# Performance work log

Hardware: AMD Instinct MI355X
Metric: run time of the kernel (lower is better)

Reference implementation:

```python
import jax, jax.numpy as jnp
import numpy as np

N_NODES = 50000
N_EDGES = 800000
NODE = 128
EDGE = 16
H = 96
OUT = 64
L = 3
BN_EPS = 1e-5


def setup_inputs() -> dict:
    key = jax.random.key(0)
    ks = iter(jax.random.split(key, 48))
    def rn(shape, s=0.05):
        return jax.random.normal(next(ks), shape, dtype=jnp.float32) * s
    inp = {
        "x": jax.random.normal(next(ks), (N_NODES, NODE), dtype=jnp.float32),
        "edge_index": jax.random.randint(next(ks), (2, N_EDGES), 0, N_NODES, dtype=jnp.int32),
        "edge_attr": jax.random.normal(next(ks), (N_EDGES, EDGE), dtype=jnp.float32),
        # GCNConv (layer 0)
        "gcn_lin_w": rn((NODE, H)), "gcn_lin_b": rn((H,)),
        "gcn_root": rn((1, H)),
        "gcn_bw1": rn((EDGE, H)), "gcn_bb1": rn((H,)),
        "gcn_bw2": rn((H, H)), "gcn_bb2": rn((H,)),
        # GINConv layers 1..L-1 (stacked)
        "gin_bw1": rn((L - 1, EDGE, H)), "gin_bb1": rn((L - 1, H)),
        "gin_bw2": rn((L - 1, H, H)), "gin_bb2": rn((L - 1, H)),
        "gin_mw1": rn((L - 1, H, H)), "gin_mb1": rn((L - 1, H)),
        "gin_mw2": rn((L - 1, H, H)), "gin_mb2": rn((L - 1, H)),
        "gin_eps": jnp.zeros((L - 1,), jnp.float32),
        # BatchNorm (eval mode, running stats)
        "bn_gamma": jnp.ones((L, H), jnp.float32),
        "bn_beta": jnp.zeros((L, H), jnp.float32),
        "bn_mean": rn((L, H)),
        "bn_var": jnp.ones((L, H), jnp.float32) + jax.random.uniform(next(ks), (L, H), dtype=jnp.float32) * 0.1,
        # head
        "fc1_w": rn((L * H, H)), "fc1_b": rn((H,)),
        "fc2_w": rn((H, OUT)), "fc2_b": rn((OUT,)),
    }
    return inp


def _bn(x, gamma, beta, mean, var):
    return (x - mean) * jax.lax.rsqrt(var + BN_EPS) * gamma + beta


def reference(x, edge_index, edge_attr,
              gcn_lin_w, gcn_lin_b, gcn_root, gcn_bw1, gcn_bb1, gcn_bw2, gcn_bb2,
              gin_bw1, gin_bb1, gin_bw2, gin_bb2, gin_mw1, gin_mb1, gin_mw2, gin_mb2, gin_eps,
              bn_gamma, bn_beta, bn_mean, bn_var,
              fc1_w, fc1_b, fc2_w, fc2_b):
    n = x.shape[0]
    row, col = edge_index[0], edge_index[1]  # source, target

    # ---- Layer 0: GCNConv with edge attributes ----
    h = x @ gcn_lin_w + gcn_lin_b                                    # [N,H]
    ee = jax.nn.relu(edge_attr @ gcn_bw1 + gcn_bb1) @ gcn_bw2 + gcn_bb2  # [E,H]
    deg = jax.ops.segment_sum(jnp.ones_like(row, dtype=h.dtype), row, num_segments=n) + 1.0
    dinv = jax.lax.rsqrt(deg)                                        # deg >= 1, no inf
    norm = dinv[row] * dinv[col]                                     # [E]
    msg = norm[:, None] * jax.nn.relu(h[row] + ee)                   # [E,H]
    agg = jax.ops.segment_sum(msg, col, num_segments=n)              # [N,H]
    h = agg + jax.nn.relu(h + gcn_root) / deg[:, None]
    h = _bn(jax.nn.relu(h), bn_gamma[0], bn_beta[0], bn_mean[0], bn_var[0])
    feats = [h]

    # ---- Layers 1..L-1: GINConv with edge attributes ----
    for i in range(L - 1):
        ee = jax.nn.relu(edge_attr @ gin_bw1[i] + gin_bb1[i]) @ gin_bw2[i] + gin_bb2[i]  # [E,H]
        agg = jax.ops.segment_sum(jax.nn.relu(h[row] + ee), col, num_segments=n)          # [N,H]
        z = (1.0 + gin_eps[i]) * h + agg
        z = jax.nn.relu(z @ gin_mw1[i] + gin_mb1[i]) @ gin_mw2[i] + gin_mb2[i]
        h = _bn(jax.nn.relu(z), bn_gamma[i + 1], bn_beta[i + 1], bn_mean[i + 1], bn_var[i + 1])
        feats.append(h)

    cat = jnp.concatenate(feats, axis=-1)                            # [N, L*H]
    y = jax.nn.relu(cat @ fc1_w + fc1_b)                             # dropout is eval-mode identity
    return y @ fc2_w + fc2_b                                         # [N, OUT]
```

## Files before the change

kernel.cpp:

```cpp
#include <hip/hip_runtime.h>


#define HH 96
#define EDGEF 16
#define CAT (3 * HH)

typedef __attribute__((ext_vector_type(8))) short bf16x8;
typedef __attribute__((ext_vector_type(4))) float f32x4;
typedef __attribute__((ext_vector_type(4))) unsigned short ubf16x4;

__device__ __forceinline__ unsigned short f2bf(float f) {
    unsigned u = __float_as_uint(f);
    u += 0x7fffu + ((u >> 16) & 1u);
    return (unsigned short)(u >> 16);
}
__device__ __forceinline__ float bf2f(unsigned short s) {
    return __uint_as_float(((unsigned)s) << 16);
}

template <int K, int F, int AMODE, int EPI>
__global__ __launch_bounds__(256) void node_gemm(
    const void* __restrict__ Aptr, int lda,
    const float* __restrict__ agg,
    const float* __restrict__ eps_arr, int li,
    const float* __restrict__ W, const float* __restrict__ bias,
    void* __restrict__ Cptr, int ldc,
    unsigned short* __restrict__ bf_copy,
    const float* __restrict__ gamma, const float* __restrict__ beta,
    const float* __restrict__ mean, const float* __restrict__ var,
    int M)
{
    constexpr int SW = ((K * 2) % 128 == 0) ? 7 : 3;
    constexpr int NFT = F / 16;
    __shared__ __align__(16) short s_wt[F * K];

    const int tid = threadIdx.x;
    const int lane = tid & 63;
    const int w = tid >> 6;
    const int lr = lane & 15;
    const int lg = lane >> 4;

    for (int idx = tid; idx < F * K; idx += 256) {
        int f = idx / K, k = idx - f * K;
        s_wt[idx ^ ((f & SW) << 3)] = (short)f2bf(W[k * F + f]);
    }
    __syncthreads();

    const int R0 = blockIdx.x * 64 + 16 * w;
    const int Ra = min(R0 + lr, M - 1);

    float e1 = 0.f;
    if (AMODE == 2) e1 = 1.f + eps_arr[li];

    f32x4 acc[NFT];
#pragma unroll
    for (int ft = 0; ft < NFT; ++ft) {
        float b = bias[16 * ft + lr];
        acc[ft][0] = b; acc[ft][1] = b; acc[ft][2] = b; acc[ft][3] = b;
    }

#pragma unroll
    for (int kt = 0; kt < K / 32; ++kt) {
        bf16x8 ae;
        if (AMODE == 0) {
            const float* ap = (const float*)Aptr + (size_t)Ra * lda + 32 * kt + 8 * lg;
            f32x4 a0 = *(const f32x4*)ap;
            f32x4 a1 = *(const f32x4*)(ap + 4);
#pragma unroll
            for (int j = 0; j < 4; ++j) {
                ae[j] = (short)f2bf(a0[j]); ae[4 + j] = (short)f2bf(a1[j]);
            }
        } else if (AMODE == 1) {
            ae = *(const bf16x8*)((const unsigned short*)Aptr + (size_t)Ra * lda + 32 * kt + 8 * lg);
        } else {
            const unsigned short* hp = (const unsigned short*)Aptr + (size_t)Ra * lda + 32 * kt + 8 * lg;
            bf16x8 h8 = *(const bf16x8*)hp;
            const float* gp = agg + (size_t)Ra * HH + 32 * kt + 8 * lg;
            f32x4 g0 = *(const f32x4*)gp;
            f32x4 g1 = *(const f32x4*)(gp + 4);
#pragma unroll
            for (int j = 0; j < 4; ++j) {
                ae[j]     = (short)f2bf(fmaf(e1, bf2f((unsigned short)h8[j]), g0[j]));
                ae[4 + j] = (short)f2bf(fmaf(e1, bf2f((unsigned short)h8[4 + j]), g1[j]));
            }
        }
#pragma unroll
        for (int ft = 0; ft < NFT; ++ft) {
            bf16x8 bw = *(const bf16x8*)&s_wt[((lr + 16 * ft) * K + 32 * kt + 8 * lg) ^ ((lr & SW) << 3)];
            acc[ft] = __builtin_amdgcn_mfma_f32_16x16x32_bf16(ae, bw, acc[ft], 0, 0, 0);
        }
    }

    float scale[NFT], shiftv[NFT];
    if (EPI == 2) {
#pragma unroll
        for (int ft = 0; ft < NFT; ++ft) {
            int col = 16 * ft + lr;
            float s = gamma[col] * rsqrtf(var[col] + 1e-5f);
            scale[ft] = s;
            shiftv[ft] = beta[col] - mean[col] * s;
        }
    }
#pragma unroll
    for (int reg = 0; reg < 4; ++reg) {
        int r = R0 + 4 * lg + reg;
        if (r < M) {
#pragma unroll
            for (int ft = 0; ft < NFT; ++ft) {
                int col = 16 * ft + lr;
                float v = acc[ft][reg];
                if (EPI == 0) {
                    ((float*)Cptr)[(size_t)r * ldc + col] = v;
                } else if (EPI == 1) {
                    ((unsigned short*)Cptr)[(size_t)r * ldc + col] = f2bf(fmaxf(v, 0.f));
                } else if (EPI == 2) {
                    float z = fmaxf(v, 0.f) * scale[ft] + shiftv[ft];
                    unsigned short zb = f2bf(z);
                    ((unsigned short*)Cptr)[(size_t)r * ldc + col] = zb;
                    bf_copy[(size_t)r * F + col] = zb;
                } else {
                    ((float*)Cptr)[(size_t)r * ldc + col] = v;
                    bf_copy[(size_t)r * F + col] = f2bf(v);
                }
            }
        }
    }
}

__global__ void init_kernel(float* __restrict__ deg, int* __restrict__ cnt, int N)
{
    int i = blockIdx.x * blockDim.x + threadIdx.x;
    if (i < N) { deg[i] = 1.f; cnt[i] = 0; }
}

__global__ void count_kernel(const int* __restrict__ row, const int* __restrict__ col,
                             float* __restrict__ deg, int* __restrict__ cnt, int E)
{
    int e = blockIdx.x * blockDim.x + threadIdx.x;
    if (e < E) {
        atomicAdd(&deg[row[e]], 1.f);
        atomicAdd(&cnt[col[e]], 1);
    }
}

__global__ void scan1_kernel(const int* __restrict__ cnt, int* __restrict__ start,
                             int* __restrict__ bsum, int N)
{
    __shared__ int s[256];
    int tid = threadIdx.x;
    int i = blockIdx.x * 256 + tid;
    int v = (i < N) ? cnt[i] : 0;
    s[tid] = v;
    __syncthreads();
#pragma unroll
    for (int off = 1; off < 256; off <<= 1) {
        int t = (tid >= off) ? s[tid - off] : 0;
        __syncthreads();
        s[tid] += t;
        __syncthreads();
    }
    if (i < N) start[i] = s[tid] - v;
    if (tid == 255) bsum[blockIdx.x] = s[255];
}

__global__ void scan2_kernel(int* __restrict__ bsum, int nb)
{
    __shared__ int s[256];
    int tid = threadIdx.x;
    int v = (tid < nb) ? bsum[tid] : 0;
    s[tid] = v;
    __syncthreads();
#pragma unroll
    for (int off = 1; off < 256; off <<= 1) {
        int t = (tid >= off) ? s[tid - off] : 0;
        __syncthreads();
        s[tid] += t;
        __syncthreads();
    }
    if (tid < nb) bsum[tid] = s[tid] - v;
}

__global__ void scan3_kernel(int* __restrict__ start, const int* __restrict__ bsum,
                             int* __restrict__ cursor,
                             const float* __restrict__ deg, float* __restrict__ dinv,
                             int N, int E)
{
    int i = blockIdx.x * blockDim.x + threadIdx.x;
    if (i < N) {
        int f = start[i] + bsum[i >> 8];
        start[i] = f;
        cursor[i] = f;
        dinv[i] = rsqrtf(deg[i]);
    } else if (i == N) {
        start[N] = E;
    }
}

__global__ void scatter_ea_kernel(const int* __restrict__ row, const int* __restrict__ col,
                                  int* __restrict__ cursor,
                                  const float* __restrict__ ea,
                                  int* __restrict__ row_sorted,
                                  unsigned short* __restrict__ eas, int E)
{
    int e = blockIdx.x * blockDim.x + threadIdx.x;
    if (e >= E) return;
    int c = col[e];
    int p = atomicAdd(&cursor[c], 1);
    row_sorted[p] = row[e];
    const float* src = ea + (size_t)e * EDGEF;
    f32x4 v0 = *(const f32x4*)(src);
    f32x4 v1 = *(const f32x4*)(src + 4);
    f32x4 v2 = *(const f32x4*)(src + 8);
    f32x4 v3 = *(const f32x4*)(src + 12);
    bf16x8 o0, o1;
#pragma unroll
    for (int j = 0; j < 4; ++j) {
        o0[j] = (short)f2bf(v0[j]); o0[4 + j] = (short)f2bf(v1[j]);
        o1[j] = (short)f2bf(v2[j]); o1[4 + j] = (short)f2bf(v3[j]);
    }
    *(bf16x8*)(eas + (size_t)p * EDGEF) = o0;
    *(bf16x8*)(eas + (size_t)p * EDGEF + 8) = o1;
}

template <bool GCN>
__global__ __launch_bounds__(256, 4) void edge_kernel(
    const unsigned short* __restrict__ ea_sorted,
    const int* __restrict__ row_sorted,
    const int* __restrict__ seg_start,
    const float* __restrict__ bw1, const float* __restrict__ bb1,
    const float* __restrict__ bw2, const float* __restrict__ bb2,
    const unsigned short* __restrict__ hbf,
    const float* __restrict__ dinv,
    float* __restrict__ agg,
    int N)
{
    __shared__ __align__(16) short s_bw2T[96][104];
    __shared__ __align__(16) short s_bw1T[96][16];
    __shared__ __align__(16) short s_t[4][16][104];
    __shared__ float s_bias[192];

    const int tid = threadIdx.x;
    const int lane = tid & 63;
    const int w = tid >> 6;
    const int lr = lane & 15;
    const int lg = lane >> 4;

    for (int idx = tid; idx < HH * HH; idx += 256) {
        int k = idx / HH, f = idx - k * HH;
        s_bw2T[f][k] = (short)f2bf(bw2[idx]);
    }
    for (int idx = tid; idx < EDGEF * HH; idx += 256) {
        int k = idx / HH, f = idx - k * HH;
        s_bw1T[f][k] = (short)f2bf(bw1[idx]);
    }
    if (tid < HH) { s_bias[tid] = bb1[tid]; s_bias[HH + tid] = bb2[tid]; }
    __syncthreads();

    const f32x4 zf = {0.f, 0.f, 0.f, 0.f};
    const int nwaves = gridDim.x * 4;

    for (int c = blockIdx.x * 4 + w; c < N; c += nwaves) {
        const int s0 = seg_start[c];
        const int s1 = seg_start[c + 1];
        float dinv_c = GCN ? dinv[c] : 1.f;

        f32x4 acc[6];
#pragma unroll
        for (int ft = 0; ft < 6; ++ft) acc[ft] = zf;

        for (int b = s0; b < s1; b += 16) {
            const int epos = b + lr;
            const bool vld = (epos < s1);
            const int epc = vld ? epos : s0;
            const int r = row_sorted[epc];

            const unsigned short* hrow = hbf + (size_t)r * HH + 24 * lg;
            bf16x8 h0 = *(const bf16x8*)(hrow);
            bf16x8 h1 = *(const bf16x8*)(hrow + 8);
            bf16x8 h2 = *(const bf16x8*)(hrow + 16);

            float nrm = GCN ? dinv[r] * dinv_c : 1.f;

            bf16x8 ae;
#pragma unroll
            for (int j = 0; j < 8; ++j) ae[j] = 0;
            if (lg < 2)
                ae = *(const bf16x8*)(ea_sorted + (size_t)epc * EDGEF + 8 * lg);

#pragma unroll
            for (int ft = 0; ft < 6; ++ft) {
                bf16x8 b1;
#pragma unroll
                for (int j = 0; j < 8; ++j) b1[j] = 0;
                if (lg < 2)
                    b1 = *(const bf16x8*)&s_bw1T[lr + 16 * ft][8 * lg];
                f32x4 tacc = __builtin_amdgcn_mfma_f32_16x16x32_bf16(ae, b1, zf, 0, 0, 0);
                float bsv = s_bias[lr + 16 * ft];
#pragma unroll
                for (int reg = 0; reg < 4; ++reg) {
                    float v = fmaxf(tacc[reg] + bsv, 0.f);
                    s_t[w][4 * lg + reg][lr + 16 * ft] = (short)f2bf(v);
                }
            }
            __builtin_amdgcn_wave_barrier();

            bf16x8 bt[3];
#pragma unroll
            for (int kt = 0; kt < 3; ++kt)
                bt[kt] = *(const bf16x8*)&s_t[w][lr][8 * lg + 32 * kt];
            __builtin_amdgcn_wave_barrier();

            *(bf16x8*)&s_t[w][lr][24 * lg]      = h0;
            *(bf16x8*)&s_t[w][lr][24 * lg + 8]  = h1;
            *(bf16x8*)&s_t[w][lr][24 * lg + 16] = h2;
            __builtin_amdgcn_wave_barrier();

#pragma unroll
            for (int ft = 0; ft < 6; ++ft) {
                f32x4 ee = zf;
#pragma unroll
                for (int kt = 0; kt < 3; ++kt) {
                    bf16x8 aw = *(const bf16x8*)&s_bw2T[lr + 16 * ft][8 * lg + 32 * kt];
                    ee = __builtin_amdgcn_mfma_f32_16x16x32_bf16(aw, bt[kt], ee, 0, 0, 0);
                }
                const int fb = 16 * ft + 4 * lg;
                f32x4 bb = *(const f32x4*)&s_bias[HH + fb];
                ubf16x4 hv = *(const ubf16x4*)&s_t[w][lr][fb];
#pragma unroll
                for (int reg = 0; reg < 4; ++reg) {
                    float m = fmaxf(bf2f(hv[reg]) + ee[reg] + bb[reg], 0.f) * nrm;
                    acc[ft][reg] += vld ? m : 0.f;
                }
            }
        }

#pragma unroll
        for (int ft = 0; ft < 6; ++ft) {
#pragma unroll
            for (int reg = 0; reg < 4; ++reg) {
                float v = acc[ft][reg];
                v += __shfl_xor(v, 1);
                v += __shfl_xor(v, 2);
                v += __shfl_xor(v, 4);
                v += __shfl_xor(v, 8);
                acc[ft][reg] = v;
            }
        }
        if (lr == 0) {
#pragma unroll
            for (int ft = 0; ft < 6; ++ft)
                *(f32x4*)&agg[(size_t)c * HH + 16 * ft + 4 * lg] = acc[ft];
        }
    }
}

__global__ void gcn_epilogue_kernel(
    const float* __restrict__ agg, const float* __restrict__ hbuf,
    const float* __restrict__ root, const float* __restrict__ deg,
    const float* __restrict__ gamma, const float* __restrict__ beta,
    const float* __restrict__ mean, const float* __restrict__ var,
    unsigned short* __restrict__ featsbf, unsigned short* __restrict__ hb, int N)
{
    int idx = blockIdx.x * blockDim.x + threadIdx.x;
    if (idx >= N * (HH / 4)) return;
    int n = idx / (HH / 4), q = idx - n * (HH / 4);
    int f0 = 4 * q;
    f32x4 a  = *(const f32x4*)&agg[(size_t)n * HH + f0];
    f32x4 h  = *(const f32x4*)&hbuf[(size_t)n * HH + f0];
    f32x4 rt = *(const f32x4*)&root[f0];
    f32x4 gm = *(const f32x4*)&gamma[f0];
    f32x4 bt = *(const f32x4*)&beta[f0];
    f32x4 mn = *(const f32x4*)&mean[f0];
    f32x4 vr = *(const f32x4*)&var[f0];
    float di = 1.f / deg[n];
    ubf16x4 o;
#pragma unroll
    for (int j = 0; j < 4; ++j) {
        float self = fmaxf(h[j] + rt[j], 0.f) * di;
        float v = fmaxf(a[j] + self, 0.f);
        v = (v - mn[j]) * rsqrtf(vr[j] + 1e-5f) * gm[j] + bt[j];
        o[j] = f2bf(v);
    }
    *(ubf16x4*)&featsbf[(size_t)n * CAT + f0] = o;
    *(ubf16x4*)&hb[(size_t)n * HH + f0] = o;
}

extern "C" void kernel_launch(void* const* d_in, const int* in_sizes, int n_in,
                              void* d_out, int out_size, void* d_ws, size_t ws_size,
                              hipStream_t stream)
{
    const float* x         = (const float*)d_in[0];
    const int*   eidx      = (const int*)d_in[1];
    const float* edge_attr = (const float*)d_in[2];
    const float* gcn_lin_w = (const float*)d_in[3];
    const float* gcn_lin_b = (const float*)d_in[4];
    const float* gcn_root  = (const float*)d_in[5];
    const float* gcn_bw1   = (const float*)d_in[6];
    const float* gcn_bb1   = (const float*)d_in[7];
    const float* gcn_bw2   = (const float*)d_in[8];
    const float* gcn_bb2   = (const float*)d_in[9];
    const float* gin_bw1   = (const float*)d_in[10];
    const float* gin_bb1   = (const float*)d_in[11];
    const float* gin_bw2   = (const float*)d_in[12];
    const float* gin_bb2   = (const float*)d_in[13];
    const float* gin_mw1   = (const float*)d_in[14];
    const float* gin_mb1   = (const float*)d_in[15];
    const float* gin_mw2   = (const float*)d_in[16];
    const float* gin_mb2   = (const float*)d_in[17];
    const float* gin_eps   = (const float*)d_in[18];
    const float* bn_gamma  = (const float*)d_in[19];
    const float* bn_beta   = (const float*)d_in[20];
    const float* bn_mean   = (const float*)d_in[21];
    const float* bn_var    = (const float*)d_in[22];
    const float* fc1_w     = (const float*)d_in[23];
    const float* fc1_b     = (const float*)d_in[24];
    const float* fc2_w     = (const float*)d_in[25];
    const float* fc2_b     = (const float*)d_in[26];
    float* out = (float*)d_out;

    const int N = in_sizes[0] / 128;
    const int E = in_sizes[1] / 2;
    const int* row = eidx;
    const int* col = eidx + E;

    char* ws = (char*)d_ws;
    float* deg        = (float*)(ws);
    float* dinv       = (float*)(ws + (size_t)256 * 1024);
    int*   seg_start  = (int*)(ws + (size_t)512 * 1024);
    int*   cursor     = (int*)(ws + (size_t)768 * 1024);
    int*   bsum       = (int*)(ws + (size_t)1024 * 1024);
    int*   row_sorted = (int*)(ws + (size_t)1088 * 1024);
    unsigned short* ea_sorted = (unsigned short*)(ws + (size_t)8 * 1024 * 1024);
    unsigned short* hb        = (unsigned short*)(ws + (size_t)34 * 1024 * 1024);
    float* hbuf   = (float*)(ws + (size_t)44 * 1024 * 1024);
    float* agg    = (float*)(ws + (size_t)64 * 1024 * 1024);
    unsigned short* featsbf = (unsigned short*)(ws + (size_t)84 * 1024 * 1024);
    unsigned short* z1bf    = (unsigned short*)(ws + (size_t)113 * 1024 * 1024);
    unsigned short* r1bf    = (unsigned short*)(ws + (size_t)123 * 1024 * 1024);

    const int ew_blocks = 1024;
    const int q_grid = (N * (HH / 4) + 255) / 256;
    const int gemm_grid = (N + 63) / 64;
    const int e_grid = (E + 255) / 256;
    const int n_grid = (N + 255) / 256;
    const int nchunks = (N + 255) / 256;

    init_kernel<<<n_grid, 256, 0, stream>>>(deg, cursor, N);
    count_kernel<<<e_grid, 256, 0, stream>>>(row, col, deg, cursor, E);
    scan1_kernel<<<nchunks, 256, 0, stream>>>(cursor, seg_start, bsum, N);
    scan2_kernel<<<1, 256, 0, stream>>>(bsum, nchunks);
    scan3_kernel<<<(N + 256) / 256, 256, 0, stream>>>(seg_start, bsum, cursor, deg, dinv, N, E);
    scatter_ea_kernel<<<e_grid, 256, 0, stream>>>(row, col, cursor, edge_attr,
                                                  row_sorted, ea_sorted, E);

    node_gemm<128, 96, 0, 3><<<gemm_grid, 256, 0, stream>>>(
        x, 128, nullptr, nullptr, 0, gcn_lin_w, gcn_lin_b,
        hbuf, HH, hb, nullptr, nullptr, nullptr, nullptr, N);
    edge_kernel<true><<<ew_blocks, 256, 0, stream>>>(
        ea_sorted, row_sorted, seg_start,
        gcn_bw1, gcn_bb1, gcn_bw2, gcn_bb2, hb, dinv, agg, N);
    gcn_epilogue_kernel<<<q_grid, 256, 0, stream>>>(
        agg, hbuf, gcn_root, deg, bn_gamma, bn_beta, bn_mean, bn_var, featsbf, hb, N);

    for (int i = 0; i < 2; ++i) {
        edge_kernel<false><<<ew_blocks, 256, 0, stream>>>(
            ea_sorted, row_sorted, seg_start,
            gin_bw1 + (size_t)i * EDGEF * HH, gin_bb1 + i * HH,
            gin_bw2 + (size_t)i * HH * HH, gin_bb2 + i * HH,
            hb, dinv, agg, N);
        node_gemm<96, 96, 2, 1><<<gemm_grid, 256, 0, stream>>>(
            hb, HH, agg, gin_eps, i,
            gin_mw1 + (size_t)i * HH * HH, gin_mb1 + i * HH,
            z1bf, HH, nullptr, nullptr, nullptr, nullptr, nullptr, N);
        node_gemm<96, 96, 1, 2><<<gemm_grid, 256, 0, stream>>>(
            z1bf, HH, nullptr, nullptr, 0,
            gin_mw2 + (size_t)i * HH * HH, gin_mb2 + i * HH,
            featsbf + (i + 1) * HH, CAT, hb,
            bn_gamma + (i + 1) * HH, bn_beta + (i + 1) * HH,
            bn_mean + (i + 1) * HH, bn_var + (i + 1) * HH, N);
    }

    node_gemm<288, 96, 1, 1><<<gemm_grid, 256, 0, stream>>>(
        featsbf, CAT, nullptr, nullptr, 0, fc1_w, fc1_b,
        r1bf, HH, nullptr, nullptr, nullptr, nullptr, nullptr, N);
    node_gemm<96, 64, 1, 0><<<gemm_grid, 256, 0, stream>>>(
        r1bf, HH, nullptr, nullptr, 0, fc2_w, fc2_b,
        out, 64, nullptr, nullptr, nullptr, nullptr, nullptr, N);
}
```

Measured before the change: 696.9 us.

## Use packed bf16 conversions and enlarge edge kernel blocks to 1024 threads

Replaces per-element manual fp32-to-bf16 rounding with packed two-element conversions via hip_bfloat162 across several kernels. Reconfigures the edge kernel to 1024-thread blocks (16 waves) with 512 blocks, so shared weights are staged once per larger block. It also folds the second bias into the MFMA accumulator init and replaces the conditional add with a masked FMA. The larger block raises LDS use per block and the launch bound of 1024,8 may limit registers per thread, which could cause spills.

```diff
diff --git a/kernel.cpp b/kernel.cpp
--- a/kernel.cpp
+++ b/kernel.cpp
@@ -1,4 +1,5 @@
 #include <hip/hip_runtime.h>
+#include <hip/hip_bf16.h>
 
 
 #define HH 96
@@ -8,6 +9,9 @@
 typedef __attribute__((ext_vector_type(8))) short bf16x8;
 typedef __attribute__((ext_vector_type(4))) float f32x4;
 typedef __attribute__((ext_vector_type(4))) unsigned short ubf16x4;
+
+typedef union { bf16x8 v; unsigned u[4]; } bfpack8;
+typedef union { ubf16x4 v; unsigned u[2]; } bfpack4;
 
 __device__ __forceinline__ unsigned short f2bf(float f) {
     unsigned u = __float_as_uint(f);
@@ -16,6 +20,10 @@
 }
 __device__ __forceinline__ float bf2f(unsigned short s) {
     return __uint_as_float(((unsigned)s) << 16);
+}
+__device__ __forceinline__ unsigned pkbf2(float lo, float hi) {
+    __hip_bfloat162 b = __float22bfloat162_rn(make_float2(lo, hi));
+    union { __hip_bfloat162 b2; unsigned u; } cv; cv.b2 = b; return cv.u;
 }
 
 template <int K, int F, int AMODE, int EPI>
@@ -66,10 +74,10 @@
             const float* ap = (const float*)Aptr + (size_t)Ra * lda + 32 * kt + 8 * lg;
             f32x4 a0 = *(const f32x4*)ap;
             f32x4 a1 = *(const f32x4*)(ap + 4);
-#pragma unroll
-            for (int j = 0; j < 4; ++j) {
-                ae[j] = (short)f2bf(a0[j]); ae[4 + j] = (short)f2bf(a1[j]);
-            }
+            bfpack8 p;
+            p.u[0] = pkbf2(a0[0], a0[1]); p.u[1] = pkbf2(a0[2], a0[3]);
+            p.u[2] = pkbf2(a1[0], a1[1]); p.u[3] = pkbf2(a1[2], a1[3]);
+            ae = p.v;
         } else if (AMODE == 1) {
             ae = *(const bf16x8*)((const unsigned short*)Aptr + (size_t)Ra * lda + 32 * kt + 8 * lg);
         } else {
@@ -78,11 +86,18 @@
             const float* gp = agg + (size_t)Ra * HH + 32 * kt + 8 * lg;
             f32x4 g0 = *(const f32x4*)gp;
             f32x4 g1 = *(const f32x4*)(gp + 4);
-#pragma unroll
-            for (int j = 0; j < 4; ++j) {
-                ae[j]     = (short)f2bf(fmaf(e1, bf2f((unsigned short)h8[j]), g0[j]));
-                ae[4 + j] = (short)f2bf(fmaf(e1, bf2f((unsigned short)h8[4 + j]), g1[j]));
-            }
+            float t0 = fmaf(e1, bf2f((unsigned short)h8[0]), g0[0]);
+            float t1 = fmaf(e1, bf2f((unsigned short)h8[1]), g0[1]);
+            float t2 = fmaf(e1, bf2f((unsigned short)h8[2]), g0[2]);
+            float t3 = fmaf(e1, bf2f((unsigned short)h8[3]), g0[3]);
+            float t4 = fmaf(e1, bf2f((unsigned short)h8[4]), g1[0]);
+            float t5 = fmaf(e1, bf2f((unsigned short)h8[5]), g1[1]);
+            float t6 = fmaf(e1, bf2f((unsigned short)h8[6]), g1[2]);
+            float t7 = fmaf(e1, bf2f((unsigned short)h8[7]), g1[3]);
+            bfpack8 p;
+            p.u[0] = pkbf2(t0, t1); p.u[1] = pkbf2(t2, t3);
+            p.u[2] = pkbf2(t4, t5); p.u[3] = pkbf2(t6, t7);
+            ae = p.v;
         }
 #pragma unroll
         for (int ft = 0; ft < NFT; ++ft) {
@@ -212,18 +227,17 @@
     f32x4 v1 = *(const f32x4*)(src + 4);
     f32x4 v2 = *(const f32x4*)(src + 8);
     f32x4 v3 = *(const f32x4*)(src + 12);
-    bf16x8 o0, o1;
-#pragma unroll
-    for (int j = 0; j < 4; ++j) {
-        o0[j] = (short)f2bf(v0[j]); o0[4 + j] = (short)f2bf(v1[j]);
-        o1[j] = (short)f2bf(v2[j]); o1[4 + j] = (short)f2bf(v3[j]);
-    }
-    *(bf16x8*)(eas + (size_t)p * EDGEF) = o0;
-    *(bf16x8*)(eas + (size_t)p * EDGEF + 8) = o1;
+    bfpack8 o0, o1;
+    o0.u[0] = pkbf2(v0[0], v0[1]); o0.u[1] = pkbf2(v0[2], v0[3]);
+    o0.u[2] = pkbf2(v1[0], v1[1]); o0.u[3] = pkbf2(v1[2], v1[3]);
+    o1.u[0] = pkbf2(v2[0], v2[1]); o1.u[1] = pkbf2(v2[2], v2[3]);
+    o1.u[2] = pkbf2(v3[0], v3[1]); o1.u[3] = pkbf2(v3[2], v3[3]);
+    *(bf16x8*)(eas + (size_t)p * EDGEF) = o0.v;
+    *(bf16x8*)(eas + (size_t)p * EDGEF + 8) = o1.v;
 }
 
 template <bool GCN>
-__global__ __launch_bounds__(256, 4) void edge_kernel(
+__global__ __launch_bounds__(1024, 8) void edge_kernel(
     const unsigned short* __restrict__ ea_sorted,
     const int* __restrict__ row_sorted,
     const int* __restrict__ seg_start,
@@ -236,7 +250,7 @@
 {
     __shared__ __align__(16) short s_bw2T[96][104];
     __shared__ __align__(16) short s_bw1T[96][16];
-    __shared__ __align__(16) short s_t[4][16][104];
+    __shared__ __align__(16) short s_t[16][16][104];
     __shared__ float s_bias[192];
 
     const int tid = threadIdx.x;
@@ -245,11 +259,11 @@
     const int lr = lane & 15;
     const int lg = lane >> 4;
 
-    for (int idx = tid; idx < HH * HH; idx += 256) {
+    for (int idx = tid; idx < HH * HH; idx += 1024) {
         int k = idx / HH, f = idx - k * HH;
         s_bw2T[f][k] = (short)f2bf(bw2[idx]);
     }
-    for (int idx = tid; idx < EDGEF * HH; idx += 256) {
+    for (int idx = tid; idx < EDGEF * HH; idx += 1024) {
         int k = idx / HH, f = idx - k * HH;
         s_bw1T[f][k] = (short)f2bf(bw1[idx]);
     }
@@ -257,9 +271,9 @@
     __syncthreads();
 
     const f32x4 zf = {0.f, 0.f, 0.f, 0.f};
-    const int nwaves = gridDim.x * 4;
-
-    for (int c = blockIdx.x * 4 + w; c < N; c += nwaves) {
+    const int nwaves = gridDim.x * 16;
+
+    for (int c = blockIdx.x * 16 + w; c < N; c += nwaves) {
         const int s0 = seg_start[c];
         const int s1 = seg_start[c + 1];
         float dinv_c = GCN ? dinv[c] : 1.f;
@@ -279,7 +293,7 @@
             bf16x8 h1 = *(const bf16x8*)(hrow + 8);
             bf16x8 h2 = *(const bf16x8*)(hrow + 16);
 
-            float nrm = GCN ? dinv[r] * dinv_c : 1.f;
+            const float msk = vld ? (GCN ? dinv[r] * dinv_c : 1.f) : 0.f;
 
             bf16x8 ae;
 #pragma unroll
@@ -296,11 +310,17 @@
                     b1 = *(const bf16x8*)&s_bw1T[lr + 16 * ft][8 * lg];
                 f32x4 tacc = __builtin_amdgcn_mfma_f32_16x16x32_bf16(ae, b1, zf, 0, 0, 0);
                 float bsv = s_bias[lr + 16 * ft];
-#pragma unroll
-                for (int reg = 0; reg < 4; ++reg) {
-                    float v = fmaxf(tacc[reg] + bsv, 0.f);
-                    s_t[w][4 * lg + reg][lr + 16 * ft] = (short)f2bf(v);
-                }
+                float v0 = fmaxf(tacc[0] + bsv, 0.f);
+                float v1 = fmaxf(tacc[1] + bsv, 0.f);
+                float v2 = fmaxf(tacc[2] + bsv, 0.f);
+                float v3 = fmaxf(tacc[3] + bsv, 0.f);
+                unsigned u01 = pkbf2(v0, v1);
+                unsigned u23 = pkbf2(v2, v3);
+                const int colf = lr + 16 * ft;
+                s_t[w][4 * lg + 0][colf] = (short)u01;
+                s_t[w][4 * lg + 1][colf] = (short)(u01 >> 16);
+                s_t[w][4 * lg + 2][colf] = (short)u23;
+                s_t[w][4 * lg + 3][colf] = (short)(u23 >> 16);
             }
             __builtin_amdgcn_wave_barrier();
 
@@ -317,19 +337,18 @@
 
 #pragma unroll
             for (int ft = 0; ft < 6; ++ft) {
-                f32x4 ee = zf;
+                const int fb = 16 * ft + 4 * lg;
+                f32x4 ee = *(const f32x4*)&s_bias[HH + fb];
 #pragma unroll
                 for (int kt = 0; kt < 3; ++kt) {
                     bf16x8 aw = *(const bf16x8*)&s_bw2T[lr + 16 * ft][8 * lg + 32 * kt];
                     ee = __builtin_amdgcn_mfma_f32_16x16x32_bf16(aw, bt[kt], ee, 0, 0, 0);
                 }
-                const int fb = 16 * ft + 4 * lg;
-                f32x4 bb = *(const f32x4*)&s_bias[HH + fb];
                 ubf16x4 hv = *(const ubf16x4*)&s_t[w][lr][fb];
 #pragma unroll
                 for (int reg = 0; reg < 4; ++reg) {
-                    float m = fmaxf(bf2f(hv[reg]) + ee[reg] + bb[reg], 0.f) * nrm;
-                    acc[ft][reg] += vld ? m : 0.f;
+                    float m = fmaxf(bf2f(hv[reg]) + ee[reg], 0.f);
+                    acc[ft][reg] = fmaf(m, msk, acc[ft][reg]);
                 }
             }
         }
@@ -373,16 +392,18 @@
     f32x4 mn = *(const f32x4*)&mean[f0];
     f32x4 vr = *(const f32x4*)&var[f0];
     float di = 1.f / deg[n];
-    ubf16x4 o;
+    float vv[4];
 #pragma unroll
     for (int j = 0; j < 4; ++j) {
         float self = fmaxf(h[j] + rt[j], 0.f) * di;
         float v = fmaxf(a[j] + self, 0.f);
-        v = (v - mn[j]) * rsqrtf(vr[j] + 1e-5f) * gm[j] + bt[j];
-        o[j] = f2bf(v);
-    }
-    *(ubf16x4*)&featsbf[(size_t)n * CAT + f0] = o;
-    *(ubf16x4*)&hb[(size_t)n * HH + f0] = o;
+        vv[j] = (v - mn[j]) * rsqrtf(vr[j] + 1e-5f) * gm[j] + bt[j];
+    }
+    bfpack4 o;
+    o.u[0] = pkbf2(vv[0], vv[1]);
+    o.u[1] = pkbf2(vv[2], vv[3]);
+    *(ubf16x4*)&featsbf[(size_t)n * CAT + f0] = o.v;
+    *(ubf16x4*)&hb[(size_t)n * HH + f0] = o.v;
 }
 
 extern "C" void kernel_launch(void* const* d_in, const int* in_sizes, int n_in,
@@ -438,7 +459,7 @@
     unsigned short* z1bf    = (unsigned short*)(ws + (size_t)113 * 1024 * 1024);
     unsigned short* r1bf    = (unsigned short*)(ws + (size_t)123 * 1024 * 1024);
 
-    const int ew_blocks = 1024;
+    const int ew_blocks = 512;
     const int q_grid = (N * (HH / 4) + 255) / 256;
     const int gemm_grid = (N + 63) / 64;
     const int e_grid = (E + 255) / 256;
@@ -456,14 +477,14 @@
     node_gemm<128, 96, 0, 3><<<gemm_grid, 256, 0, stream>>>(
         x, 128, nullptr, nullptr, 0, gcn_lin_w, gcn_lin_b,
         hbuf, HH, hb, nullptr, nullptr, nullptr, nullptr, N);
-    edge_kernel<true><<<ew_blocks, 256, 0, stream>>>(
+    edge_kernel<true><<<ew_blocks, 1024, 0, stream>>>(
         ea_sorted, row_sorted, seg_start,
         gcn_bw1, gcn_bb1, gcn_bw2, gcn_bb2, hb, dinv, agg, N);
     gcn_epilogue_kernel<<<q_grid, 256, 0, stream>>>(
         agg, hbuf, gcn_root, deg, bn_gamma, bn_beta, bn_mean, bn_var, featsbf, hb, N);
 
     for (int i = 0; i < 2; ++i) {
-        edge_kernel<false><<<ew_blocks, 256, 0, stream>>>(
+        edge_kernel<false><<<ew_blocks, 1024, 0, stream>>>(
             ea_sorted, row_sorted, seg_start,
             gin_bw1 + (size_t)i * EDGEF * HH, gin_bb1 + i * HH,
             gin_bw2 + (size_t)i * HH * HH, gin_bb2 + i * HH,
```

Measured after the change: 717.7 us. 1.03x slower.
